# Optimization experiments

Measured on AMD Instinct MI355X. Metric: run time of the kernel, lower is better.

The kernel has to match this reference:

```python
import jax, jax.numpy as jnp
import numpy as np

N_NODES = 500_000
N_EDGES = 16_000_000
F_IN = 4
C = 4


def setup_inputs() -> dict:
    key = jax.random.key(0)
    ks = jax.random.split(key, 8)
    x = jax.random.normal(ks[0], (N_NODES, F_IN), dtype=jnp.float32)
    edge_index = jax.random.randint(ks[1], (2, N_EDGES), 0, N_NODES, dtype=jnp.int32)
    node = 1000  # node id whose incident edges are scored
    # GCNConv weights (PyG lin weight is [out,in]; math is x @ W with W=[in,out]) + separate bias
    W1 = jax.random.normal(ks[2], (F_IN, C), dtype=jnp.float32) * 0.5
    b1 = jnp.zeros((C,), dtype=jnp.float32)
    W2 = jax.random.normal(ks[3], (C, C), dtype=jnp.float32) * 0.5
    b2 = jnp.zeros((C,), dtype=jnp.float32)
    Wr = jax.random.normal(ks[4], (C, 1), dtype=jnp.float32) * 0.5
    br = jnp.zeros((1,), dtype=jnp.float32)
    return {"x": x, "edge_index": edge_index, "node": node,
            "W1": W1, "b1": b1, "W2": W2, "b2": b2, "Wr": Wr, "br": br}


def reference(x, edge_index, node, W1, b1, W2, b2, Wr, br):
    n = x.shape[0]
    src, dst = edge_index[0], edge_index[1]
    # GCN normalization with added self-loops (PyG gcn_norm, edge_weight=1)
    loop = jnp.arange(n, dtype=src.dtype)
    srcl = jnp.concatenate([src, loop])  # [E+N]
    dstl = jnp.concatenate([dst, loop])
    deg = jax.ops.segment_sum(jnp.ones(srcl.shape[0], dtype=x.dtype), dstl, num_segments=n)
    dinv = jnp.where(deg > 0, jax.lax.rsqrt(deg), jnp.zeros_like(deg))
    norm = (dinv[srcl] * dinv[dstl])[:, None]  # [E+N, 1]

    def gcn_conv(h, W, b):
        hW = h @ W                                  # tiny GEMM [N,C]
        msg = hW[srcl] * norm                       # edge gather + normalize [E+N, C]
        return jax.ops.segment_sum(msg, dstl, num_segments=n) + b  # scatter-add

    h = jax.nn.relu(gcn_conv(x, W1, b1))
    h = jax.nn.relu(gcn_conv(h, W2, b2))

    # Edges incident to `node`; softmax restricted to them (others masked out)
    mask = (src == node) | (dst == node)            # [E]
    targets = jnp.where(src == node, dst, src)      # other endpoint (node itself for self-loop)
    logits = (h[targets] @ Wr + br)[:, 0]           # [E]
    neg = jnp.finfo(logits.dtype).min
    score = jax.nn.softmax(jnp.where(mask, logits, neg))  # masked entries -> 0
    targets_out = jnp.where(mask, targets, -1)
    return score, targets_out
```

## Files before the change

kernel.cpp:

```cpp
#include <hip/hip_runtime.h>

#define CAP_I   65536
#define CAP_S1  (1 << 18)
#define CAP_L2  (1 << 20)
#define CAP_L1  (1 << 22)
#define LBUF    2560
#define NWMAX   15680

typedef unsigned int uint;
typedef float vfloat4 __attribute__((ext_vector_type(4)));

__global__ void k_passA(const int4* __restrict__ src4, const int4* __restrict__ dst4, int nvec,
                        const int* __restrict__ nodep,
                        int* __restrict__ cnts, int* __restrict__ le, int* __restrict__ lt) {
    int node = *nodep;
    int stride = gridDim.x * blockDim.x;
    for (int v = blockIdx.x * blockDim.x + threadIdx.x; v < nvec; v += stride) {
        int4 s4 = src4[v];
        int4 d4 = dst4[v];
        int ss[4] = {s4.x, s4.y, s4.z, s4.w};
        int dd[4] = {d4.x, d4.y, d4.z, d4.w};
#pragma unroll
        for (int k = 0; k < 4; k++) {
            if (ss[k] == node || dd[k] == node) {
                int t = (ss[k] == node) ? dd[k] : ss[k];
                int pos = atomicAdd(&cnts[0], 1);
                if (pos < CAP_I) { le[pos] = v * 4 + k; lt[pos] = t; }
            }
        }
    }
}

__global__ void k_markT(const int* __restrict__ cnts, const int* __restrict__ lt,
                        uint* __restrict__ bmT, uint* __restrict__ bmS1,
                        uint* __restrict__ bmS0,
                        int* __restrict__ cnts_w, int* __restrict__ s1list,
                        int* __restrict__ deg, float4* __restrict__ acc1,
                        float4* __restrict__ acc2) {
    int n = cnts[0]; if (n > CAP_I) n = CAP_I;
    const float4 z4 = make_float4(0.f, 0.f, 0.f, 0.f);
    for (int i = threadIdx.x; i < n; i += blockDim.x) {
        int t = lt[i];
        uint bit = 1u << (t & 31);
        atomicOr(&bmT[t >> 5], bit);
        uint old = atomicOr(&bmS1[t >> 5], bit);
        if (!(old & bit)) {
            atomicOr(&bmS0[t >> 5], bit);
            deg[t] = 0; acc1[t] = z4; acc2[t] = z4;
            int p = atomicAdd(&cnts_w[2], 1);
            if (p < CAP_S1) s1list[p] = t;
        }
    }
}

__global__ __launch_bounds__(512) void k_passB(
        const int* __restrict__ src, const int4* __restrict__ dst4, int nvec, int NW,
        const uint* __restrict__ bmT, uint* __restrict__ bmS1, uint* __restrict__ bmS0,
        int* __restrict__ cnts, int* __restrict__ l2s, int* __restrict__ l2t,
        int* __restrict__ s1list,
        int* __restrict__ deg, float4* __restrict__ acc1, float4* __restrict__ acc2) {
    __shared__ uint lT[NWMAX];
    __shared__ int bes[LBUF], bet[LBUF], bs1[LBUF];
    __shared__ int lcE, lcS, gbE, gbS;
    for (int i = threadIdx.x; i < NW; i += blockDim.x) lT[i] = bmT[i];
    if (threadIdx.x == 0) { lcE = 0; lcS = 0; }
    __syncthreads();
    const float4 z4 = make_float4(0.f, 0.f, 0.f, 0.f);
    int stride = gridDim.x * blockDim.x;
    for (int v = blockIdx.x * blockDim.x + threadIdx.x; v < nvec; v += stride) {
        int4 d4 = dst4[v];
        int dd[4] = {d4.x, d4.y, d4.z, d4.w};
#pragma unroll
        for (int k = 0; k < 4; k++) {
            int d = dd[k];
            if ((lT[d >> 5] >> (d & 31)) & 1u) {
                int s = src[v * 4 + k];
                int p = atomicAdd(&lcE, 1);
                if (p < LBUF) { bes[p] = s; bet[p] = d; }
                else {
                    int g = atomicAdd(&cnts[1], 1);
                    if (g < CAP_L2) { l2s[g] = s; l2t[g] = d; }
                }
                uint bit = 1u << (s & 31);
                uint old = atomicOr(&bmS1[s >> 5], bit);
                if (!(old & bit)) {
                    atomicOr(&bmS0[s >> 5], bit);
                    deg[s] = 0; acc1[s] = z4; acc2[s] = z4;
                    int q = atomicAdd(&lcS, 1);
                    if (q < LBUF) bs1[q] = s;
                    else {
                        int g = atomicAdd(&cnts[2], 1);
                        if (g < CAP_S1) s1list[g] = s;
                    }
                }
            }
        }
    }
    __syncthreads();
    int nE = min(lcE, LBUF), nS = min(lcS, LBUF);
    if (threadIdx.x == 0) {
        gbE = (nE > 0) ? atomicAdd(&cnts[1], nE) : 0;
        gbS = (nS > 0) ? atomicAdd(&cnts[2], nS) : 0;
    }
    __syncthreads();
    for (int i = threadIdx.x; i < nE; i += blockDim.x) {
        int pos = gbE + i;
        if (pos < CAP_L2) { l2s[pos] = bes[i]; l2t[pos] = bet[i]; }
    }
    for (int i = threadIdx.x; i < nS; i += blockDim.x) {
        int pos = gbS + i;
        if (pos < CAP_S1) s1list[pos] = bs1[i];
    }
}

__global__ __launch_bounds__(512) void k_passC(
        const int* __restrict__ src, const int4* __restrict__ dst4, int nvec, int NW,
        const uint* __restrict__ bmS1, uint* __restrict__ bmS0,
        int* __restrict__ cnts, int* __restrict__ l1s, int* __restrict__ l1t,
        int* __restrict__ deg) {
    __shared__ uint lS1[NWMAX];
    __shared__ int lbs[LBUF], lbt[LBUF];
    __shared__ int lcnt, gbase;
    for (int i = threadIdx.x; i < NW; i += blockDim.x) lS1[i] = bmS1[i];
    if (threadIdx.x == 0) lcnt = 0;
    __syncthreads();
    int stride = gridDim.x * blockDim.x;
    for (int v = blockIdx.x * blockDim.x + threadIdx.x; v < nvec; v += stride) {
        int4 d4 = dst4[v];
        int dd[4] = {d4.x, d4.y, d4.z, d4.w};
#pragma unroll
        for (int k = 0; k < 4; k++) {
            int d = dd[k];
            if ((lS1[d >> 5] >> (d & 31)) & 1u) {
                int s = src[v * 4 + k];
                uint bit = 1u << (s & 31);
                uint old = atomicOr(&bmS0[s >> 5], bit);
                if (!(old & bit)) deg[s] = 0;
                int p = atomicAdd(&lcnt, 1);
                if (p < LBUF) { lbs[p] = s; lbt[p] = d; }
                else {
                    int g = atomicAdd(&cnts[3], 1);
                    if (g < CAP_L1) { l1s[g] = s; l1t[g] = d; }
                }
            }
        }
    }
    __syncthreads();
    int n = min(lcnt, LBUF);
    if (threadIdx.x == 0) gbase = (n > 0) ? atomicAdd(&cnts[3], n) : 0;
    __syncthreads();
    for (int i = threadIdx.x; i < n; i += blockDim.x) {
        int pos = gbase + i;
        if (pos < CAP_L1) { l1s[pos] = lbs[i]; l1t[pos] = lbt[i]; }
    }
}

__global__ __launch_bounds__(256) void k_passD(
        const int4* __restrict__ dst4, int nvec,
        const uint* __restrict__ bmS0, int* __restrict__ deg,
        vfloat4* __restrict__ out_score4, vfloat4* __restrict__ out_tgt4) {
    const vfloat4 zero = {0.f, 0.f, 0.f, 0.f};
    const vfloat4 neg1 = {-1.f, -1.f, -1.f, -1.f};
    int stride = gridDim.x * blockDim.x;
    for (int v = blockIdx.x * blockDim.x + threadIdx.x; v < nvec; v += stride) {
        int4 d4 = dst4[v];
        __builtin_nontemporal_store(zero, &out_score4[v]);
        __builtin_nontemporal_store(neg1, &out_tgt4[v]);
        int dd[4] = {d4.x, d4.y, d4.z, d4.w};
#pragma unroll
        for (int k = 0; k < 4; k++) {
            int d = dd[k];
            if ((bmS0[d >> 5] >> (d & 31)) & 1u) atomicAdd(&deg[d], 1);
        }
    }
}

__global__ void k_conv1(const int* __restrict__ cnts, const int* __restrict__ l1s,
                        const int* __restrict__ l1t, const float* __restrict__ x,
                        const float* __restrict__ W1, const int* __restrict__ deg,
                        float* __restrict__ acc1) {
    int n = cnts[3]; if (n > CAP_L1) n = CAP_L1;
    int stride = gridDim.x * blockDim.x;
    for (int j = blockIdx.x * blockDim.x + threadIdx.x; j < n; j += stride) {
        int s = l1s[j], d = l1t[j];
        float4 xv = *(const float4*)(x + (size_t)s * 4);
        float dis = rsqrtf((float)deg[s] + 1.0f);
        float o0 = (xv.x * W1[0] + xv.y * W1[4] + xv.z * W1[8]  + xv.w * W1[12]) * dis;
        float o1 = (xv.x * W1[1] + xv.y * W1[5] + xv.z * W1[9]  + xv.w * W1[13]) * dis;
        float o2 = (xv.x * W1[2] + xv.y * W1[6] + xv.z * W1[10] + xv.w * W1[14]) * dis;
        float o3 = (xv.x * W1[3] + xv.y * W1[7] + xv.z * W1[11] + xv.w * W1[15]) * dis;
        float* a = acc1 + (size_t)d * 4;
        atomicAdd(a + 0, o0); atomicAdd(a + 1, o1);
        atomicAdd(a + 2, o2); atomicAdd(a + 3, o3);
    }
}

__global__ __launch_bounds__(1024) void k_tail(
        const int* __restrict__ cnts, const int* __restrict__ s1list,
        const int* __restrict__ l2s, const int* __restrict__ l2t,
        const int* __restrict__ le, const int* __restrict__ lt,
        const float* __restrict__ x, const float* __restrict__ W1,
        const float* __restrict__ b1, const float* __restrict__ W2,
        const float* __restrict__ b2, const float* __restrict__ Wr,
        const float* __restrict__ br, const int* __restrict__ deg,
        const float* __restrict__ acc1, float* __restrict__ acc2,
        float* __restrict__ gB, float* __restrict__ z,
        float* __restrict__ out_score, float* __restrict__ out_tgt) {
    int tid = threadIdx.x;
    int n2 = cnts[2]; if (n2 > CAP_S1) n2 = CAP_S1;
    for (int j = tid; j < n2; j += blockDim.x) {
        int i = s1list[j];
        float di = rsqrtf((float)deg[i] + 1.0f);
        float4 xv = *(const float4*)(x + (size_t)i * 4);
        float4 a  = *(const float4*)(acc1 + (size_t)i * 4);
        float w0 = xv.x * W1[0] + xv.y * W1[4] + xv.z * W1[8]  + xv.w * W1[12];
        float w1 = xv.x * W1[1] + xv.y * W1[5] + xv.z * W1[9]  + xv.w * W1[13];
        float w2 = xv.x * W1[2] + xv.y * W1[6] + xv.z * W1[10] + xv.w * W1[14];
        float w3 = xv.x * W1[3] + xv.y * W1[7] + xv.z * W1[11] + xv.w * W1[15];
        float h0 = fmaxf((a.x + w0 * di) * di + b1[0], 0.f);
        float h1 = fmaxf((a.y + w1 * di) * di + b1[1], 0.f);
        float h2 = fmaxf((a.z + w2 * di) * di + b1[2], 0.f);
        float h3 = fmaxf((a.w + w3 * di) * di + b1[3], 0.f);
        float4 o;
        o.x = (h0 * W2[0] + h1 * W2[4] + h2 * W2[8]  + h3 * W2[12]) * di;
        o.y = (h0 * W2[1] + h1 * W2[5] + h2 * W2[9]  + h3 * W2[13]) * di;
        o.z = (h0 * W2[2] + h1 * W2[6] + h2 * W2[10] + h3 * W2[14]) * di;
        o.w = (h0 * W2[3] + h1 * W2[7] + h2 * W2[11] + h3 * W2[15]) * di;
        *(float4*)(gB + (size_t)i * 4) = o;
    }
    __syncthreads();
    int nL2 = cnts[1]; if (nL2 > CAP_L2) nL2 = CAP_L2;
    for (int j = tid; j < nL2; j += blockDim.x) {
        int s = l2s[j], t = l2t[j];
        float4 g = *(const float4*)(gB + (size_t)s * 4);
        float* a = acc2 + (size_t)t * 4;
        atomicAdd(a + 0, g.x); atomicAdd(a + 1, g.y);
        atomicAdd(a + 2, g.z); atomicAdd(a + 3, g.w);
    }
    __syncthreads();
    int nI = cnts[0]; if (nI > CAP_I) nI = CAP_I;
    for (int j = tid; j < nI; j += blockDim.x) {
        int t = lt[j];
        float di = rsqrtf((float)deg[t] + 1.0f);
        float4 a = *(const float4*)(acc2 + (size_t)t * 4);
        float4 g = *(const float4*)(gB + (size_t)t * 4);
        float h0 = fmaxf((a.x + g.x) * di + b2[0], 0.f);
        float h1 = fmaxf((a.y + g.y) * di + b2[1], 0.f);
        float h2 = fmaxf((a.z + g.z) * di + b2[2], 0.f);
        float h3 = fmaxf((a.w + g.w) * di + b2[3], 0.f);
        z[t] = h0 * Wr[0] + h1 * Wr[1] + h2 * Wr[2] + h3 * Wr[3] + br[0];
    }
    __syncthreads();
    if (tid == 0) {
        float m = -3.402823466e+38f;
        for (int k = 0; k < nI; k++) m = fmaxf(m, z[lt[k]]);
        float ssum = 0.f;
        for (int k = 0; k < nI; k++) ssum += __expf(z[lt[k]] - m);
        float inv = (ssum > 0.f) ? 1.f / ssum : 0.f;
        for (int k = 0; k < nI; k++) {
            out_score[le[k]] = __expf(z[lt[k]] - m) * inv;
            out_tgt[le[k]]   = (float)lt[k];
        }
    }
}

extern "C" void kernel_launch(void* const* d_in, const int* in_sizes, int n_in,
                              void* d_out, int out_size, void* d_ws, size_t ws_size,
                              hipStream_t stream) {
    const float* x  = (const float*)d_in[0];
    const int*   ei = (const int*)d_in[1];
    const int*   nodep = (const int*)d_in[2];
    const float* W1 = (const float*)d_in[3];
    const float* b1 = (const float*)d_in[4];
    const float* W2 = (const float*)d_in[5];
    const float* b2 = (const float*)d_in[6];
    const float* Wr = (const float*)d_in[7];
    const float* br = (const float*)d_in[8];

    const int N = in_sizes[0] / 4;
    const int E = in_sizes[1] / 2;
    const int nvec = E / 4;
    const int NW = (N + 31) / 32;
    const int* src = ei;
    const int* dst = ei + E;

    char* ws = (char*)d_ws;
    size_t off = 0;
    auto alloc = [&](size_t bytes) { char* p = ws + off; off = (off + bytes + 255) & ~(size_t)255; return p; };
    char* zero_base = ws;
    uint*  bmT    = (uint*) alloc((size_t)NW * 4);
    uint*  bmS1   = (uint*) alloc((size_t)NW * 4);
    uint*  bmS0   = (uint*) alloc((size_t)NW * 4);
    int*   cnts   = (int*)  alloc(256);
    size_t zero_len = off;
    int*   deg    = (int*)  alloc((size_t)N * 4);
    float* acc1   = (float*)alloc((size_t)N * 16);
    float* acc2   = (float*)alloc((size_t)N * 16);
    float* gB     = (float*)alloc((size_t)N * 16);
    float* z      = (float*)alloc((size_t)N * 4);
    int*   le     = (int*)  alloc((size_t)CAP_I * 4);
    int*   lt     = (int*)  alloc((size_t)CAP_I * 4);
    int*   s1list = (int*)  alloc((size_t)CAP_S1 * 4);
    int*   l2s    = (int*)  alloc((size_t)CAP_L2 * 4);
    int*   l2t    = (int*)  alloc((size_t)CAP_L2 * 4);
    int*   l1s    = (int*)  alloc((size_t)CAP_L1 * 4);
    int*   l1t    = (int*)  alloc((size_t)CAP_L1 * 4);

    float* out_score = (float*)d_out;
    float* out_tgt   = out_score + E;

    int edgeBlocksA = (nvec + 255) / 256;
    if (edgeBlocksA > 2048) edgeBlocksA = 2048;

    (void)hipMemsetAsync(zero_base, 0, zero_len, stream);

    k_passA<<<edgeBlocksA, 256, 0, stream>>>((const int4*)src, (const int4*)dst, nvec, nodep,
                                             cnts, le, lt);
    k_markT<<<1, 256, 0, stream>>>(cnts, lt, bmT, bmS1, bmS0, cnts, s1list,
                                   deg, (float4*)acc1, (float4*)acc2);
    k_passB<<<512, 512, 0, stream>>>(src, (const int4*)dst, nvec, NW, bmT, bmS1, bmS0,
                                     cnts, l2s, l2t, s1list,
                                     deg, (float4*)acc1, (float4*)acc2);
    k_passC<<<512, 512, 0, stream>>>(src, (const int4*)dst, nvec, NW, bmS1, bmS0,
                                     cnts, l1s, l1t, deg);
    k_passD<<<2048, 256, 0, stream>>>((const int4*)dst, nvec, bmS0, deg,
                                      (vfloat4*)out_score, (vfloat4*)out_tgt);
    k_conv1<<<256, 256, 0, stream>>>(cnts, l1s, l1t, x, W1, deg, acc1);
    k_tail<<<1, 1024, 0, stream>>>(cnts, s1list, l2s, l2t, le, lt, x, W1, b1, W2, b2,
                                   Wr, br, deg, acc1, acc2, gB, z, out_score, out_tgt);
}
```

Baseline: 300.3 us.

## Replace full LDS bitmaps with coarse summary bitmaps and fold markT into passA

```diff
diff --git a/kernel.cpp b/kernel.cpp
--- a/kernel.cpp
+++ b/kernel.cpp
@@ -4,15 +4,24 @@
 #define CAP_S1  (1 << 18)
 #define CAP_L2  (1 << 20)
 #define CAP_L1  (1 << 22)
-#define LBUF    2560
-#define NWMAX   15680
+#define LBUF_B  512
+#define LBUF_C  1024
+#define CBT_W   977
+#define CBS_W   1954
 
 typedef unsigned int uint;
 typedef float vfloat4 __attribute__((ext_vector_type(4)));
 
 __global__ void k_passA(const int4* __restrict__ src4, const int4* __restrict__ dst4, int nvec,
                         const int* __restrict__ nodep,
-                        int* __restrict__ cnts, int* __restrict__ le, int* __restrict__ lt) {
+                        int* __restrict__ cnts, int* __restrict__ le, int* __restrict__ lt,
+                        uint* __restrict__ bmT, uint* __restrict__ bmS1,
+                        uint* __restrict__ bmS0,
+                        uint* __restrict__ cbmT, uint* __restrict__ cbmS1,
+                        int* __restrict__ s1list,
+                        int* __restrict__ deg, float4* __restrict__ acc1,
+                        float4* __restrict__ acc2) {
+    const float4 z4 = make_float4(0.f, 0.f, 0.f, 0.f);
     int node = *nodep;
     int stride = gridDim.x * blockDim.x;
     for (int v = blockIdx.x * blockDim.x + threadIdx.x; v < nvec; v += stride) {
@@ -26,43 +35,33 @@
                 int t = (ss[k] == node) ? dd[k] : ss[k];
                 int pos = atomicAdd(&cnts[0], 1);
                 if (pos < CAP_I) { le[pos] = v * 4 + k; lt[pos] = t; }
+                uint bit = 1u << (t & 31);
+                atomicOr(&bmT[t >> 5], bit);
+                atomicOr(&cbmT[t >> 9], 1u << ((t >> 4) & 31));
+                uint old = atomicOr(&bmS1[t >> 5], bit);
+                if (!(old & bit)) {
+                    atomicOr(&bmS0[t >> 5], bit);
+                    atomicOr(&cbmS1[t >> 8], 1u << ((t >> 3) & 31));
+                    deg[t] = 0; acc1[t] = z4; acc2[t] = z4;
+                    int p = atomicAdd(&cnts[2], 1);
+                    if (p < CAP_S1) s1list[p] = t;
+                }
             }
         }
     }
 }
 
-__global__ void k_markT(const int* __restrict__ cnts, const int* __restrict__ lt,
-                        uint* __restrict__ bmT, uint* __restrict__ bmS1,
-                        uint* __restrict__ bmS0,
-                        int* __restrict__ cnts_w, int* __restrict__ s1list,
-                        int* __restrict__ deg, float4* __restrict__ acc1,
-                        float4* __restrict__ acc2) {
-    int n = cnts[0]; if (n > CAP_I) n = CAP_I;
-    const float4 z4 = make_float4(0.f, 0.f, 0.f, 0.f);
-    for (int i = threadIdx.x; i < n; i += blockDim.x) {
-        int t = lt[i];
-        uint bit = 1u << (t & 31);
-        atomicOr(&bmT[t >> 5], bit);
-        uint old = atomicOr(&bmS1[t >> 5], bit);
-        if (!(old & bit)) {
-            atomicOr(&bmS0[t >> 5], bit);
-            deg[t] = 0; acc1[t] = z4; acc2[t] = z4;
-            int p = atomicAdd(&cnts_w[2], 1);
-            if (p < CAP_S1) s1list[p] = t;
-        }
-    }
-}
-
-__global__ __launch_bounds__(512) void k_passB(
-        const int* __restrict__ src, const int4* __restrict__ dst4, int nvec, int NW,
-        const uint* __restrict__ bmT, uint* __restrict__ bmS1, uint* __restrict__ bmS0,
+__global__ __launch_bounds__(256) void k_passB(
+        const int* __restrict__ src, const int4* __restrict__ dst4, int nvec,
+        const uint* __restrict__ cbmT, const uint* __restrict__ bmT,
+        uint* __restrict__ bmS1, uint* __restrict__ bmS0, uint* __restrict__ cbmS1,
         int* __restrict__ cnts, int* __restrict__ l2s, int* __restrict__ l2t,
         int* __restrict__ s1list,
         int* __restrict__ deg, float4* __restrict__ acc1, float4* __restrict__ acc2) {
-    __shared__ uint lT[NWMAX];
-    __shared__ int bes[LBUF], bet[LBUF], bs1[LBUF];
+    __shared__ uint lcb[CBT_W];
+    __shared__ int bes[LBUF_B], bet[LBUF_B], bs1[LBUF_B];
     __shared__ int lcE, lcS, gbE, gbS;
-    for (int i = threadIdx.x; i < NW; i += blockDim.x) lT[i] = bmT[i];
+    for (int i = threadIdx.x; i < CBT_W; i += blockDim.x) lcb[i] = cbmT[i];
     if (threadIdx.x == 0) { lcE = 0; lcS = 0; }
     __syncthreads();
     const float4 z4 = make_float4(0.f, 0.f, 0.f, 0.f);
@@ -73,31 +72,30 @@
 #pragma unroll
         for (int k = 0; k < 4; k++) {
             int d = dd[k];
-            if ((lT[d >> 5] >> (d & 31)) & 1u) {
-                int s = src[v * 4 + k];
-                int p = atomicAdd(&lcE, 1);
-                if (p < LBUF) { bes[p] = s; bet[p] = d; }
-                else {
-                    int g = atomicAdd(&cnts[1], 1);
-                    if (g < CAP_L2) { l2s[g] = s; l2t[g] = d; }
-                }
-                uint bit = 1u << (s & 31);
-                uint old = atomicOr(&bmS1[s >> 5], bit);
-                if (!(old & bit)) {
-                    atomicOr(&bmS0[s >> 5], bit);
-                    deg[s] = 0; acc1[s] = z4; acc2[s] = z4;
-                    int q = atomicAdd(&lcS, 1);
-                    if (q < LBUF) bs1[q] = s;
-                    else {
-                        int g = atomicAdd(&cnts[2], 1);
-                        if (g < CAP_S1) s1list[g] = s;
+            if ((lcb[d >> 9] >> ((d >> 4) & 31)) & 1u) {
+                if ((bmT[d >> 5] >> (d & 31)) & 1u) {
+                    int s = src[v * 4 + k];
+                    int p = atomicAdd(&lcE, 1);
+                    if (p < LBUF_B) { bes[p] = s; bet[p] = d; }
+                    else { int g = atomicAdd(&cnts[1], 1);
+                           if (g < CAP_L2) { l2s[g] = s; l2t[g] = d; } }
+                    uint bit = 1u << (s & 31);
+                    uint old = atomicOr(&bmS1[s >> 5], bit);
+                    if (!(old & bit)) {
+                        atomicOr(&bmS0[s >> 5], bit);
+                        atomicOr(&cbmS1[s >> 8], 1u << ((s >> 3) & 31));
+                        deg[s] = 0; acc1[s] = z4; acc2[s] = z4;
+                        int q = atomicAdd(&lcS, 1);
+                        if (q < LBUF_B) bs1[q] = s;
+                        else { int g = atomicAdd(&cnts[2], 1);
+                               if (g < CAP_S1) s1list[g] = s; }
                     }
                 }
             }
         }
     }
     __syncthreads();
-    int nE = min(lcE, LBUF), nS = min(lcS, LBUF);
+    int nE = min(lcE, LBUF_B), nS = min(lcS, LBUF_B);
     if (threadIdx.x == 0) {
         gbE = (nE > 0) ? atomicAdd(&cnts[1], nE) : 0;
         gbS = (nS > 0) ? atomicAdd(&cnts[2], nS) : 0;
@@ -113,15 +111,16 @@
     }
 }
 
-__global__ __launch_bounds__(512) void k_passC(
-        const int* __restrict__ src, const int4* __restrict__ dst4, int nvec, int NW,
-        const uint* __restrict__ bmS1, uint* __restrict__ bmS0,
+__global__ __launch_bounds__(256) void k_passC(
+        const int* __restrict__ src, const int4* __restrict__ dst4, int nvec,
+        const uint* __restrict__ cbmS1, const uint* __restrict__ bmS1,
+        uint* __restrict__ bmS0,
         int* __restrict__ cnts, int* __restrict__ l1s, int* __restrict__ l1t,
         int* __restrict__ deg) {
-    __shared__ uint lS1[NWMAX];
-    __shared__ int lbs[LBUF], lbt[LBUF];
+    __shared__ uint lcb[CBS_W];
+    __shared__ int lbs[LBUF_C], lbt[LBUF_C];
     __shared__ int lcnt, gbase;
-    for (int i = threadIdx.x; i < NW; i += blockDim.x) lS1[i] = bmS1[i];
+    for (int i = threadIdx.x; i < CBS_W; i += blockDim.x) lcb[i] = cbmS1[i];
     if (threadIdx.x == 0) lcnt = 0;
     __syncthreads();
     int stride = gridDim.x * blockDim.x;
@@ -131,22 +130,22 @@
 #pragma unroll
         for (int k = 0; k < 4; k++) {
             int d = dd[k];
-            if ((lS1[d >> 5] >> (d & 31)) & 1u) {
-                int s = src[v * 4 + k];
-                uint bit = 1u << (s & 31);
-                uint old = atomicOr(&bmS0[s >> 5], bit);
-                if (!(old & bit)) deg[s] = 0;
-                int p = atomicAdd(&lcnt, 1);
-                if (p < LBUF) { lbs[p] = s; lbt[p] = d; }
-                else {
-                    int g = atomicAdd(&cnts[3], 1);
-                    if (g < CAP_L1) { l1s[g] = s; l1t[g] = d; }
+            if ((lcb[d >> 8] >> ((d >> 3) & 31)) & 1u) {
+                if ((bmS1[d >> 5] >> (d & 31)) & 1u) {
+                    int s = src[v * 4 + k];
+                    uint bit = 1u << (s & 31);
+                    uint old = atomicOr(&bmS0[s >> 5], bit);
+                    if (!(old & bit)) deg[s] = 0;
+                    int p = atomicAdd(&lcnt, 1);
+                    if (p < LBUF_C) { lbs[p] = s; lbt[p] = d; }
+                    else { int g = atomicAdd(&cnts[3], 1);
+                           if (g < CAP_L1) { l1s[g] = s; l1t[g] = d; } }
                 }
             }
         }
     }
     __syncthreads();
-    int n = min(lcnt, LBUF);
+    int n = min(lcnt, LBUF_C);
     if (threadIdx.x == 0) gbase = (n > 0) ? atomicAdd(&cnts[3], n) : 0;
     __syncthreads();
     for (int i = threadIdx.x; i < n; i += blockDim.x) {
@@ -291,6 +290,8 @@
     uint*  bmT    = (uint*) alloc((size_t)NW * 4);
     uint*  bmS1   = (uint*) alloc((size_t)NW * 4);
     uint*  bmS0   = (uint*) alloc((size_t)NW * 4);
+    uint*  cbmT   = (uint*) alloc((size_t)CBT_W * 4);
+    uint*  cbmS1  = (uint*) alloc((size_t)CBS_W * 4);
     int*   cnts   = (int*)  alloc(256);
     size_t zero_len = off;
     int*   deg    = (int*)  alloc((size_t)N * 4);
@@ -315,15 +316,14 @@
     (void)hipMemsetAsync(zero_base, 0, zero_len, stream);
 
     k_passA<<<edgeBlocksA, 256, 0, stream>>>((const int4*)src, (const int4*)dst, nvec, nodep,
-                                             cnts, le, lt);
-    k_markT<<<1, 256, 0, stream>>>(cnts, lt, bmT, bmS1, bmS0, cnts, s1list,
-                                   deg, (float4*)acc1, (float4*)acc2);
-    k_passB<<<512, 512, 0, stream>>>(src, (const int4*)dst, nvec, NW, bmT, bmS1, bmS0,
-                                     cnts, l2s, l2t, s1list,
-                                     deg, (float4*)acc1, (float4*)acc2);
-    k_passC<<<512, 512, 0, stream>>>(src, (const int4*)dst, nvec, NW, bmS1, bmS0,
-                                     cnts, l1s, l1t, deg);
-    k_passD<<<2048, 256, 0, stream>>>((const int4*)dst, nvec, bmS0, deg,
+                                             cnts, le, lt, bmT, bmS1, bmS0, cbmT, cbmS1,
+                                             s1list, deg, (float4*)acc1, (float4*)acc2);
+    k_passB<<<2048, 256, 0, stream>>>(src, (const int4*)dst, nvec, cbmT, bmT,
+                                      bmS1, bmS0, cbmS1, cnts, l2s, l2t, s1list,
+                                      deg, (float4*)acc1, (float4*)acc2);
+    k_passC<<<2048, 256, 0, stream>>>(src, (const int4*)dst, nvec, cbmS1, bmS1, bmS0,
+                                      cnts, l1s, l1t, deg);
+    k_passD<<<4096, 256, 0, stream>>>((const int4*)dst, nvec, bmS0, deg,
                                       (vfloat4*)out_score, (vfloat4*)out_tgt);
     k_conv1<<<256, 256, 0, stream>>>(cnts, l1s, l1t, x, W1, deg, acc1);
     k_tail<<<1, 1024, 0, stream>>>(cnts, s1list, l2s, l2t, le, lt, x, W1, b1, W2, b2,
```

After: 281.3 us. 1.07x faster.
